# Performance work log

Measured on AMD Instinct MI355X. Metric: run time of the kernel, lower is better.

## Reference

```python
import jax, jax.numpy as jnp
import numpy as np

HID, OUT, D = 256, 64, 128
N_ITEM, N_USER, E = 100000, 50000, 800000


def sage_conv(x_src, x_dst, src, dst, w_l, b_l, w_r, n_dst):
    # PyG SAGEConv (mean aggr): out = lin_l(mean_j x_src[j]) + lin_r(x_dst)
    msg = x_src[src]                                        # [E, d_src] gather
    agg = jax.ops.segment_sum(msg, dst, num_segments=n_dst)  # [n_dst, d_src]
    cnt = jax.ops.segment_sum(jnp.ones((src.shape[0],), x_src.dtype), dst,
                              num_segments=n_dst)
    mean = agg / jnp.clip(cnt, 1.0, None)[:, None]
    return mean @ w_l + b_l + x_dst @ w_r


def setup_inputs() -> dict:
    key = jax.random.key(0)
    ks = jax.random.split(key, 16)
    sc = lambda d: 1.0 / np.sqrt(d)
    inp = {
        "x_item": jax.random.normal(ks[0], (N_ITEM, D), jnp.float32),
        "x_user": jax.random.normal(ks[1], (N_USER, D), jnp.float32),
        "ei_ii_src": jax.random.randint(ks[2], (E,), 0, N_ITEM),
        "ei_ii_dst": jax.random.randint(ks[3], (E,), 0, N_ITEM),
        "ei_iu_src": jax.random.randint(ks[4], (E,), 0, N_ITEM),
        "ei_iu_dst": jax.random.randint(ks[5], (E,), 0, N_USER),
        # conv1: item->item, in (D, D) -> HID
        "w_l1": jax.random.normal(ks[6], (D, HID), jnp.float32) * sc(D),
        "b1": jnp.zeros((HID,), jnp.float32),
        "w_r1": jax.random.normal(ks[7], (D, HID), jnp.float32) * sc(D),
        # conv2: (item D, user D) -> HID
        "w_l2": jax.random.normal(ks[8], (D, HID), jnp.float32) * sc(D),
        "b2": jnp.zeros((HID,), jnp.float32),
        "w_r2": jax.random.normal(ks[9], (D, HID), jnp.float32) * sc(D),
        # conv3: (item HID, user HID) -> HID
        "w_l3": jax.random.normal(ks[10], (HID, HID), jnp.float32) * sc(HID),
        "b3": jnp.zeros((HID,), jnp.float32),
        "w_r3": jax.random.normal(ks[11], (HID, HID), jnp.float32) * sc(HID),
        # final linear HID -> OUT
        "w_lin": jax.random.normal(ks[12], (HID, OUT), jnp.float32) * sc(HID),
        "b_lin": jnp.zeros((OUT,), jnp.float32),
    }
    return inp


def reference(x_item, x_user, ei_ii_src, ei_ii_dst, ei_iu_src, ei_iu_dst,
              w_l1, b1, w_r1, w_l2, b2, w_r2, w_l3, b3, w_r3, w_lin, b_lin):
    item_x = jax.nn.relu(sage_conv(x_item, x_item, ei_ii_src, ei_ii_dst,
                                   w_l1, b1, w_r1, N_ITEM))
    user_x = jax.nn.relu(sage_conv(x_item, x_user, ei_iu_src, ei_iu_dst,
                                   w_l2, b2, w_r2, N_USER))
    user_x = jax.nn.relu(sage_conv(item_x, user_x, ei_iu_src, ei_iu_dst,
                                   w_l3, b3, w_r3, N_USER))
    return user_x @ w_lin + b_lin
```

## Files before the change

### kernel.cpp

```cpp
#include <hip/hip_runtime.h>
#include <hip/hip_bf16.h>

#define N_ITEM 100000
#define N_USER 50000
#define D_IN   128
#define HID    256
#define OUT_D  64
#define CAP    64

#define SCB   782
#define CVIB  2048
#define CVUB  1024
#define PKB   136
#define PREP_GRID (SCB + CVIB + CVUB + PKB)

#define C2B   391
#define A3B   3125

typedef __attribute__((ext_vector_type(8))) short bf16x8;
typedef __attribute__((ext_vector_type(4))) float f32x4;

__device__ inline float b2f(unsigned int h) {
    union { unsigned int u; float f; } c; c.u = h << 16; return c.f;
}
__device__ inline unsigned short f2b(float f) {
    unsigned int u = __builtin_bit_cast(unsigned int, f);
    u += 0x7fff + ((u >> 16) & 1);
    return (unsigned short)(u >> 16);
}

__device__ inline void pack_unit(const float* __restrict__ wl,
                                 const float* __restrict__ wr,
                                 int K, int NCv, unsigned short* __restrict__ dst,
                                 int u)
{
    int kb = u / NCv, col = u - kb * NCv;
    int colp = col ^ (kb & 7);
    unsigned short tmp[8];
    #pragma unroll
    for (int j = 0; j < 8; ++j) {
        int k = kb * 8 + j;
        float w = (k < K) ? wl[(size_t)k * NCv + col]
                          : wr[(size_t)(k - K) * NCv + col];
        tmp[j] = f2b(w);
    }
    *(uint4*)&dst[((size_t)kb * NCv + colp) * 8] = *(const uint4*)tmp;
}

__global__ __launch_bounds__(256) void prep_kernel(
    const int* __restrict__ ii_src, const int* __restrict__ ii_dst,
    const int* __restrict__ iu_src, const int* __restrict__ iu_dst,
    int* __restrict__ cur_i, int* __restrict__ cur_u,
    int* __restrict__ slot_ii, int* __restrict__ slot_iu, int E,
    const float* __restrict__ x_item, const float* __restrict__ x_user,
    unsigned short* __restrict__ Acat1, unsigned short* __restrict__ Acat2,
    const float* __restrict__ wl1, const float* __restrict__ wr1,
    const float* __restrict__ wl2, const float* __restrict__ wr2,
    const float* __restrict__ wl3, const float* __restrict__ wr3,
    const float* __restrict__ wlin,
    unsigned short* __restrict__ Wp1, unsigned short* __restrict__ Wp2,
    unsigned short* __restrict__ Wp3, unsigned short* __restrict__ Wpl)
{
    int b = blockIdx.x;
    if (b < SCB) {
        int t = b * 256 + threadIdx.x;
        int e4 = t * 4;
        if (e4 + 3 < E) {
            int4 di = *(const int4*)&ii_dst[e4];
            int4 si = *(const int4*)&ii_src[e4];
            int4 du = *(const int4*)&iu_dst[e4];
            int4 su = *(const int4*)&iu_src[e4];
            int p0 = atomicAdd(&cur_i[di.x], 1);
            int p1 = atomicAdd(&cur_i[di.y], 1);
            int p2 = atomicAdd(&cur_i[di.z], 1);
            int p3 = atomicAdd(&cur_i[di.w], 1);
            int q0 = atomicAdd(&cur_u[du.x], 1);
            int q1 = atomicAdd(&cur_u[du.y], 1);
            int q2 = atomicAdd(&cur_u[du.z], 1);
            int q3 = atomicAdd(&cur_u[du.w], 1);
            if (p0 < CAP) slot_ii[di.x * CAP + p0] = si.x;
            if (p1 < CAP) slot_ii[di.y * CAP + p1] = si.y;
            if (p2 < CAP) slot_ii[di.z * CAP + p2] = si.z;
            if (p3 < CAP) slot_ii[di.w * CAP + p3] = si.w;
            if (q0 < CAP) slot_iu[du.x * CAP + q0] = su.x;
            if (q1 < CAP) slot_iu[du.y * CAP + q1] = su.y;
            if (q2 < CAP) slot_iu[du.z * CAP + q2] = su.z;
            if (q3 < CAP) slot_iu[du.w * CAP + q3] = su.w;
        } else {
            for (int e = e4; e < E; ++e) {
                int d0 = ii_dst[e], s0 = ii_src[e];
                int p = atomicAdd(&cur_i[d0], 1);
                if (p < CAP) slot_ii[d0 * CAP + p] = s0;
                int d1 = iu_dst[e], s1 = iu_src[e];
                int q = atomicAdd(&cur_u[d1], 1);
                if (q < CAP) slot_iu[d1 * CAP + q] = s1;
            }
        }
    } else if (b < SCB + CVIB) {
        const int STR = CVIB * 256;
        for (int u = (b - SCB) * 256 + threadIdx.x; u < N_ITEM * 32; u += STR) {
            int row = u >> 5, c4 = (u & 31) * 4;
            float4 v = *(const float4*)&x_item[(size_t)row * 128 + c4];
            ushort4 o;
            o.x = f2b(v.x); o.y = f2b(v.y); o.z = f2b(v.z); o.w = f2b(v.w);
            *(ushort4*)&Acat1[(size_t)row * 256 + 128 + c4] = o;
        }
    } else if (b < SCB + CVIB + CVUB) {
        const int STR = CVUB * 256;
        for (int u = (b - SCB - CVIB) * 256 + threadIdx.x; u < N_USER * 32; u += STR) {
            int row = u >> 5, c4 = (u & 31) * 4;
            float4 v = *(const float4*)&x_user[(size_t)row * 128 + c4];
            ushort4 o;
            o.x = f2b(v.x); o.y = f2b(v.y); o.z = f2b(v.z); o.w = f2b(v.w);
            *(ushort4*)&Acat2[(size_t)row * 256 + 128 + c4] = o;
        }
    } else {
        int t = (b - SCB - CVIB - CVUB) * 256 + threadIdx.x;
        if (t < 8192)       pack_unit(wl1, wr1, 128, 256, Wp1, t);
        else if (t < 16384) pack_unit(wl2, wr2, 128, 256, Wp2, t - 8192);
        else if (t < 32768) pack_unit(wl3, wr3, 256, 256, Wp3, t - 16384);
        else if (t < 34816) pack_unit(wlin, wlin, 256, 64, Wpl, t - 32768);
    }
}

__global__ __launch_bounds__(256) void agg12_kernel(
    const unsigned short* __restrict__ xsrc,
    const int* __restrict__ slot_ii, const int* __restrict__ cur_i,
    const int* __restrict__ slot_iu, const int* __restrict__ cur_u,
    unsigned short* __restrict__ Acat1, unsigned short* __restrict__ Acat2)
{
    int b = blockIdx.x;
    int sub = threadIdx.x >> 5;
    const int* sl; int num; unsigned short* dst;
    if (b < 12500) {
        int row = b * 8 + sub;
        sl  = slot_ii + (size_t)row * CAP;
        num = min(cur_i[row], CAP);
        dst = Acat1 + (size_t)row * 256;
    } else {
        int row = (b - 12500) * 8 + sub;
        sl  = slot_iu + (size_t)row * CAP;
        num = min(cur_u[row], CAP);
        dst = Acat2 + (size_t)row * 256;
    }
    int hl = threadIdx.x & 31;
    const unsigned short* xb = xsrc + hl * 4;
    float acc[4] = {};

    int j = 0;
    for (; j + 8 <= num; j += 8) {
        int s[8];
        #pragma unroll
        for (int u = 0; u < 8; ++u) s[u] = sl[j + u];
        uint2 v[8];
        #pragma unroll
        for (int u = 0; u < 8; ++u)
            v[u] = *(const uint2*)(xb + (size_t)s[u] * 256);
        #pragma unroll
        for (int u = 0; u < 8; ++u) {
            acc[0] += b2f(v[u].x & 0xffffu);
            acc[1] += b2f(v[u].x >> 16);
            acc[2] += b2f(v[u].y & 0xffffu);
            acc[3] += b2f(v[u].y >> 16);
        }
    }
    for (; j < num; ++j) {
        uint2 v = *(const uint2*)(xb + (size_t)sl[j] * 256);
        acc[0] += b2f(v.x & 0xffffu);
        acc[1] += b2f(v.x >> 16);
        acc[2] += b2f(v.y & 0xffffu);
        acc[3] += b2f(v.y >> 16);
    }

    float sc = 1.0f / fmaxf((float)num, 1.0f);
    uint2 w;
    w.x = (unsigned int)f2b(acc[0] * sc) | ((unsigned int)f2b(acc[1] * sc) << 16);
    w.y = (unsigned int)f2b(acc[2] * sc) | ((unsigned int)f2b(acc[3] * sc) << 16);
    *(uint2*)(dst + hl * 4) = w;
}

template <int NC, int WM, int WN, bool OUT_BF16, bool RELU>
__device__ __forceinline__ void gemm_body(
    int bid,
    const unsigned short* __restrict__ A, int lda,
    const unsigned short* __restrict__ Wp,
    const float* __restrict__ bias,
    void* __restrict__ Cout, int ldc, int col_off,
    int nrows, int nkt)
{
    constexpr int BM = 128;
    constexpr int MR = WM / 16, NR = WN / 16;
    constexpr int NWC = NC / WN;
    __shared__ unsigned short As[BM * 64];
    __shared__ unsigned short Bs[64 * NC];

    const int tid  = threadIdx.x;
    const int wave = tid >> 6;
    const int lane = tid & 63;
    const int row0 = bid * BM;
    const int wr = wave / NWC;
    const int wc = wave % NWC;

    f32x4 acc[MR][NR];
    #pragma unroll
    for (int m = 0; m < MR; ++m)
        #pragma unroll
        for (int n = 0; n < NR; ++n)
            acc[m][n] = (f32x4){0.f, 0.f, 0.f, 0.f};

    for (int kt = 0; kt < nkt; ++kt) {
        #pragma unroll
        for (int c = 0; c < 2; ++c) {
            int i = wave * 2 + c;
            int rl = 8 * i + (lane >> 3);
            int kc = (lane & 7) ^ (lane >> 3);
            const unsigned short* g =
                A + (size_t)(row0 + rl) * lda + kt * 64 + kc * 8;
            __builtin_amdgcn_global_load_lds(
                (const __attribute__((address_space(1))) void*)g,
                (__attribute__((address_space(3))) void*)(As + i * 512), 16, 0, 0);
        }
        constexpr int BCALLS = (64 * NC * 2) / 1024;
        constexpr int PW = BCALLS / 8;
        #pragma unroll
        for (int c = 0; c < PW; ++c) {
            int j = wave * PW + c;
            const unsigned short* g =
                Wp + (size_t)kt * (8 * NC * 8) + (size_t)j * 512 + lane * 8;
            __builtin_amdgcn_global_load_lds(
                (const __attribute__((address_space(1))) void*)g,
                (__attribute__((address_space(3))) void*)(Bs + j * 512), 16, 0, 0);
        }
        __syncthreads();

        #pragma unroll
        for (int kk = 0; kk < 2; ++kk) {
            bf16x8 af[MR], bfr[NR];
            #pragma unroll
            for (int m = 0; m < MR; ++m) {
                int row = wr * WM + m * 16 + (lane & 15);
                int kc = ((kk * 4) + (lane >> 4)) ^ (lane & 7);
                af[m] = *(const bf16x8*)(As + row * 64 + kc * 8);
            }
            #pragma unroll
            for (int n = 0; n < NR; ++n) {
                int kb = kk * 4 + (lane >> 4);
                int col = (wc * WN + n * 16 + (lane & 15)) ^ (kb & 7);
                bfr[n] = *(const bf16x8*)(Bs + (kb * NC + col) * 8);
            }
            #pragma unroll
            for (int m = 0; m < MR; ++m)
                #pragma unroll
                for (int n = 0; n < NR; ++n)
                    acc[m][n] = __builtin_amdgcn_mfma_f32_16x16x32_bf16(
                        af[m], bfr[n], acc[m][n], 0, 0, 0);
        }
        __syncthreads();
    }

    #pragma unroll
    for (int n = 0; n < NR; ++n) {
        int col = wc * WN + n * 16 + (lane & 15);
        float bv = bias[col];
        #pragma unroll
        for (int m = 0; m < MR; ++m) {
            #pragma unroll
            for (int j = 0; j < 4; ++j) {
                int row = row0 + wr * WM + m * 16 + (lane >> 4) * 4 + j;
                if (row < nrows) {
                    float v = acc[m][n][j] + bv;
                    if (RELU) v = fmaxf(v, 0.f);
                    if (OUT_BF16)
                        ((unsigned short*)Cout)[(size_t)row * ldc + col_off + col] = f2b(v);
                    else
                        ((float*)Cout)[(size_t)row * ldc + col_off + col] = v;
                }
            }
        }
    }
}

template <int NC, int WM, int WN, bool OUT_BF16, bool RELU>
__global__ __launch_bounds__(512) void gemm_mfma(
    const unsigned short* __restrict__ A, int lda,
    const unsigned short* __restrict__ Wp,
    const float* __restrict__ bias,
    void* __restrict__ Cout, int ldc, int col_off,
    int nrows, int nkt)
{
    gemm_body<NC, WM, WN, OUT_BF16, RELU>(blockIdx.x, A, lda, Wp, bias,
                                          Cout, ldc, col_off, nrows, nkt);
}

__global__ __launch_bounds__(512) void conv2_agg3_kernel(
    const unsigned short* __restrict__ Acat2,
    const unsigned short* __restrict__ Wp2,
    const float* __restrict__ b2,
    unsigned short* __restrict__ Acat3,
    const unsigned short* __restrict__ item_x,
    const int* __restrict__ slot_iu, const int* __restrict__ cur_u)
{
    if (blockIdx.x < C2B) {
        gemm_body<256, 64, 64, true, true>(blockIdx.x, Acat2, 256, Wp2, b2,
                                           Acat3, 512, 256, N_USER, 4);
        return;
    }
    int b = blockIdx.x - C2B;
    int row = b * 16 + (threadIdx.x >> 5);
    int hl = threadIdx.x & 31;
    const int* sl = slot_iu + (size_t)row * CAP;
    int num = min(cur_u[row], CAP);
    const unsigned short* xb = item_x + hl * 8;
    float acc[8] = {};

    int j = 0;
    for (; j + 8 <= num; j += 8) {
        int s[8];
        #pragma unroll
        for (int u = 0; u < 8; ++u) s[u] = sl[j + u];
        uint4 v[8];
        #pragma unroll
        for (int u = 0; u < 8; ++u)
            v[u] = *(const uint4*)(xb + (size_t)s[u] * 256);
        #pragma unroll
        for (int u = 0; u < 8; ++u) {
            acc[0] += b2f(v[u].x & 0xffffu);
            acc[1] += b2f(v[u].x >> 16);
            acc[2] += b2f(v[u].y & 0xffffu);
            acc[3] += b2f(v[u].y >> 16);
            acc[4] += b2f(v[u].z & 0xffffu);
            acc[5] += b2f(v[u].z >> 16);
            acc[6] += b2f(v[u].w & 0xffffu);
            acc[7] += b2f(v[u].w >> 16);
        }
    }
    for (; j < num; ++j) {
        uint4 v = *(const uint4*)(xb + (size_t)sl[j] * 256);
        acc[0] += b2f(v.x & 0xffffu);
        acc[1] += b2f(v.x >> 16);
        acc[2] += b2f(v.y & 0xffffu);
        acc[3] += b2f(v.y >> 16);
        acc[4] += b2f(v.z & 0xffffu);
        acc[5] += b2f(v.z >> 16);
        acc[6] += b2f(v.w & 0xffffu);
        acc[7] += b2f(v.w >> 16);
    }

    float sc = 1.0f / fmaxf((float)num, 1.0f);
    uint4 w;
    w.x = (unsigned int)f2b(acc[0] * sc) | ((unsigned int)f2b(acc[1] * sc) << 16);
    w.y = (unsigned int)f2b(acc[2] * sc) | ((unsigned int)f2b(acc[3] * sc) << 16);
    w.z = (unsigned int)f2b(acc[4] * sc) | ((unsigned int)f2b(acc[5] * sc) << 16);
    w.w = (unsigned int)f2b(acc[6] * sc) | ((unsigned int)f2b(acc[7] * sc) << 16);
    *(uint4*)(Acat3 + (size_t)row * 512 + hl * 8) = w;
}

extern "C" void kernel_launch(void* const* d_in, const int* in_sizes, int n_in,
                              void* d_out, int out_size, void* d_ws, size_t ws_size,
                              hipStream_t stream)
{
    const float* x_item = (const float*)d_in[0];
    const float* x_user = (const float*)d_in[1];
    const int* ii_src   = (const int*)d_in[2];
    const int* ii_dst   = (const int*)d_in[3];
    const int* iu_src   = (const int*)d_in[4];
    const int* iu_dst   = (const int*)d_in[5];
    const float* w_l1 = (const float*)d_in[6];
    const float* b1   = (const float*)d_in[7];
    const float* w_r1 = (const float*)d_in[8];
    const float* w_l2 = (const float*)d_in[9];
    const float* b2   = (const float*)d_in[10];
    const float* w_r2 = (const float*)d_in[11];
    const float* w_l3 = (const float*)d_in[12];
    const float* b3   = (const float*)d_in[13];
    const float* w_r3 = (const float*)d_in[14];
    const float* w_lin = (const float*)d_in[15];
    const float* b_lin = (const float*)d_in[16];
    float* out = (float*)d_out;

    const int E = in_sizes[2];
    const int NIP = 100096;
    const int NUP = 50048;

    int* cur_i   = (int*)d_ws;
    int* cur_u   = cur_i + 100352;
    int* slot_ii = cur_u + 50176;
    int* slot_iu = slot_ii + (size_t)N_ITEM * CAP;

    unsigned short* Acat1  = (unsigned short*)(slot_iu + (size_t)N_USER * CAP);
    unsigned short* item_x = Acat1  + (size_t)NIP * 256;
    unsigned short* Acat2  = item_x + (size_t)NIP * 256;
    unsigned short* Acat3  = Acat2  + (size_t)NUP * 256;
    unsigned short* ux3    = Acat3  + (size_t)NUP * 512;
    unsigned short* Wp1    = ux3    + (size_t)NUP * 256;
    unsigned short* Wp2    = Wp1 + 65536;
    unsigned short* Wp3    = Wp2 + 65536;
    unsigned short* Wpl    = Wp3 + 131072;

    hipMemsetAsync(cur_i, 0, (size_t)150528 * 4, stream);

    prep_kernel<<<PREP_GRID, 256, 0, stream>>>(
        ii_src, ii_dst, iu_src, iu_dst, cur_i, cur_u, slot_ii, slot_iu, E,
        x_item, x_user, Acat1, Acat2,
        w_l1, w_r1, w_l2, w_r2, w_l3, w_r3, w_lin,
        Wp1, Wp2, Wp3, Wpl);

    agg12_kernel<<<18750, 256, 0, stream>>>(
        Acat1 + 128, slot_ii, cur_i, slot_iu, cur_u, Acat1, Acat2);

    gemm_mfma<256, 64, 64, true, true><<<NIP / 128, 512, 0, stream>>>(
        Acat1, 256, Wp1, b1, item_x, 256, 0, N_ITEM, 4);

    conv2_agg3_kernel<<<C2B + A3B, 512, 0, stream>>>(
        Acat2, Wp2, b2, Acat3, item_x, slot_iu, cur_u);

    gemm_mfma<256, 64, 64, true, true><<<NUP / 128, 512, 0, stream>>>(
        Acat3, 512, Wp3, b3, ux3, 256, 0, N_USER, 8);

    gemm_mfma<64, 16, 64, false, false><<<NUP / 128, 512, 0, stream>>>(
        ux3, 256, Wpl, b_lin, out, 64, 0, N_USER, 4);
}
```

Measured before the change: 383.0 us.

## Restage pipeline to overlap iu scatter with item aggregation and conv1 with user aggregation

Splits the edge scatter into two stages. The item-user scatter now runs in the same launch as the item-item mean aggregation, and the item-user aggregation runs alongside the conv1 GEMM. Independent work is packed into shared grids so each launch has more concurrent blocks and there is less idle tail between dependent kernels. Launch count stays the same, but block sizes move to 512 threads. Packing GEMM blocks with gather blocks in one grid can cause imbalance or resource contention between the two kinds of blocks.

```diff
diff --git a/kernel.cpp b/kernel.cpp
--- a/kernel.cpp
+++ b/kernel.cpp
@@ -8,14 +8,23 @@
 #define OUT_D  64
 #define CAP    64
 
-#define SCB   782
-#define CVIB  2048
-#define CVUB  1024
-#define PKB   136
-#define PREP_GRID (SCB + CVIB + CVUB + PKB)
+#define S1B   391
+#define CV1B  1024
+#define CV2B  512
+#define PK1B  68
+#define G1 (S1B + CV1B + CV2B + PK1B)
+
+#define S2B   391
+#define A1B   6250
+#define G2 (S2B + A1B)
+
+#define C1B   782
+#define A2B   3125
+#define G3 (C1B + A2B)
 
 #define C2B   391
 #define A3B   3125
+#define G4 (C2B + A3B)
 
 typedef __attribute__((ext_vector_type(8))) short bf16x8;
 typedef __attribute__((ext_vector_type(4))) float f32x4;
@@ -27,6 +36,69 @@
     unsigned int u = __builtin_bit_cast(unsigned int, f);
     u += 0x7fff + ((u >> 16) & 1);
     return (unsigned short)(u >> 16);
+}
+
+__device__ __forceinline__ void scatter_body(
+    const int* __restrict__ src, const int* __restrict__ dstl,
+    int* __restrict__ cur, int* __restrict__ slot, int E, int t)
+{
+    int e4 = t * 4;
+    if (e4 + 3 < E) {
+        int4 d = *(const int4*)&dstl[e4];
+        int4 s = *(const int4*)&src[e4];
+        int p0 = atomicAdd(&cur[d.x], 1);
+        int p1 = atomicAdd(&cur[d.y], 1);
+        int p2 = atomicAdd(&cur[d.z], 1);
+        int p3 = atomicAdd(&cur[d.w], 1);
+        if (p0 < CAP) slot[d.x * CAP + p0] = s.x;
+        if (p1 < CAP) slot[d.y * CAP + p1] = s.y;
+        if (p2 < CAP) slot[d.z * CAP + p2] = s.z;
+        if (p3 < CAP) slot[d.w * CAP + p3] = s.w;
+    } else {
+        for (int e = e4; e < E; ++e) {
+            int d0 = dstl[e], s0 = src[e];
+            int p = atomicAdd(&cur[d0], 1);
+            if (p < CAP) slot[d0 * CAP + p] = s0;
+        }
+    }
+}
+
+__device__ __forceinline__ void agg_mean128_body(
+    const unsigned short* __restrict__ xsrc,
+    const int* __restrict__ sl, int num, int hl,
+    unsigned short* __restrict__ dstrow)
+{
+    const unsigned short* xb = xsrc + hl * 4;
+    float acc[4] = {};
+    int j = 0;
+    for (; j + 8 <= num; j += 8) {
+        int s[8];
+        #pragma unroll
+        for (int u = 0; u < 8; ++u) s[u] = sl[j + u];
+        uint2 v[8];
+        #pragma unroll
+        for (int u = 0; u < 8; ++u)
+            v[u] = *(const uint2*)(xb + (size_t)s[u] * 256);
+        #pragma unroll
+        for (int u = 0; u < 8; ++u) {
+            acc[0] += b2f(v[u].x & 0xffffu);
+            acc[1] += b2f(v[u].x >> 16);
+            acc[2] += b2f(v[u].y & 0xffffu);
+            acc[3] += b2f(v[u].y >> 16);
+        }
+    }
+    for (; j < num; ++j) {
+        uint2 v = *(const uint2*)(xb + (size_t)sl[j] * 256);
+        acc[0] += b2f(v.x & 0xffffu);
+        acc[1] += b2f(v.x >> 16);
+        acc[2] += b2f(v.y & 0xffffu);
+        acc[3] += b2f(v.y >> 16);
+    }
+    float sc = 1.0f / fmaxf((float)num, 1.0f);
+    uint2 w;
+    w.x = (unsigned int)f2b(acc[0] * sc) | ((unsigned int)f2b(acc[1] * sc) << 16);
+    w.y = (unsigned int)f2b(acc[2] * sc) | ((unsigned int)f2b(acc[3] * sc) << 16);
+    *(uint2*)(dstrow + hl * 4) = w;
 }
 
 __device__ inline void pack_unit(const float* __restrict__ wl,
@@ -47,11 +119,9 @@
     *(uint4*)&dst[((size_t)kb * NCv + colp) * 8] = *(const uint4*)tmp;
 }
 
-__global__ __launch_bounds__(256) void prep_kernel(
+__global__ __launch_bounds__(512) void prep1_kernel(
     const int* __restrict__ ii_src, const int* __restrict__ ii_dst,
-    const int* __restrict__ iu_src, const int* __restrict__ iu_dst,
-    int* __restrict__ cur_i, int* __restrict__ cur_u,
-    int* __restrict__ slot_ii, int* __restrict__ slot_iu, int E,
+    int* __restrict__ cur_i, int* __restrict__ slot_ii, int E,
     const float* __restrict__ x_item, const float* __restrict__ x_user,
     unsigned short* __restrict__ Acat1, unsigned short* __restrict__ Acat2,
     const float* __restrict__ wl1, const float* __restrict__ wr1,
@@ -62,52 +132,20 @@
     unsigned short* __restrict__ Wp3, unsigned short* __restrict__ Wpl)
 {
     int b = blockIdx.x;
-    if (b < SCB) {
-        int t = b * 256 + threadIdx.x;
-        int e4 = t * 4;
-        if (e4 + 3 < E) {
-            int4 di = *(const int4*)&ii_dst[e4];
-            int4 si = *(const int4*)&ii_src[e4];
-            int4 du = *(const int4*)&iu_dst[e4];
-            int4 su = *(const int4*)&iu_src[e4];
-            int p0 = atomicAdd(&cur_i[di.x], 1);
-            int p1 = atomicAdd(&cur_i[di.y], 1);
-            int p2 = atomicAdd(&cur_i[di.z], 1);
-            int p3 = atomicAdd(&cur_i[di.w], 1);
-            int q0 = atomicAdd(&cur_u[du.x], 1);
-            int q1 = atomicAdd(&cur_u[du.y], 1);
-            int q2 = atomicAdd(&cur_u[du.z], 1);
-            int q3 = atomicAdd(&cur_u[du.w], 1);
-            if (p0 < CAP) slot_ii[di.x * CAP + p0] = si.x;
-            if (p1 < CAP) slot_ii[di.y * CAP + p1] = si.y;
-            if (p2 < CAP) slot_ii[di.z * CAP + p2] = si.z;
-            if (p3 < CAP) slot_ii[di.w * CAP + p3] = si.w;
-            if (q0 < CAP) slot_iu[du.x * CAP + q0] = su.x;
-            if (q1 < CAP) slot_iu[du.y * CAP + q1] = su.y;
-            if (q2 < CAP) slot_iu[du.z * CAP + q2] = su.z;
-            if (q3 < CAP) slot_iu[du.w * CAP + q3] = su.w;
-        } else {
-            for (int e = e4; e < E; ++e) {
-                int d0 = ii_dst[e], s0 = ii_src[e];
-                int p = atomicAdd(&cur_i[d0], 1);
-                if (p < CAP) slot_ii[d0 * CAP + p] = s0;
-                int d1 = iu_dst[e], s1 = iu_src[e];
-                int q = atomicAdd(&cur_u[d1], 1);
-                if (q < CAP) slot_iu[d1 * CAP + q] = s1;
-            }
-        }
-    } else if (b < SCB + CVIB) {
-        const int STR = CVIB * 256;
-        for (int u = (b - SCB) * 256 + threadIdx.x; u < N_ITEM * 32; u += STR) {
+    if (b < S1B) {
+        scatter_body(ii_src, ii_dst, cur_i, slot_ii, E, b * 512 + threadIdx.x);
+    } else if (b < S1B + CV1B) {
+        const int STR = CV1B * 512;
+        for (int u = (b - S1B) * 512 + threadIdx.x; u < N_ITEM * 32; u += STR) {
             int row = u >> 5, c4 = (u & 31) * 4;
             float4 v = *(const float4*)&x_item[(size_t)row * 128 + c4];
             ushort4 o;
             o.x = f2b(v.x); o.y = f2b(v.y); o.z = f2b(v.z); o.w = f2b(v.w);
             *(ushort4*)&Acat1[(size_t)row * 256 + 128 + c4] = o;
         }
-    } else if (b < SCB + CVIB + CVUB) {
-        const int STR = CVUB * 256;
-        for (int u = (b - SCB - CVIB) * 256 + threadIdx.x; u < N_USER * 32; u += STR) {
+    } else if (b < S1B + CV1B + CV2B) {
+        const int STR = CV2B * 512;
+        for (int u = (b - S1B - CV1B) * 512 + threadIdx.x; u < N_USER * 32; u += STR) {
             int row = u >> 5, c4 = (u & 31) * 4;
             float4 v = *(const float4*)&x_user[(size_t)row * 128 + c4];
             ushort4 o;
@@ -115,7 +153,7 @@
             *(ushort4*)&Acat2[(size_t)row * 256 + 128 + c4] = o;
         }
     } else {
-        int t = (b - SCB - CVIB - CVUB) * 256 + threadIdx.x;
+        int t = (b - S1B - CV1B - CV2B) * 512 + threadIdx.x;
         if (t < 8192)       pack_unit(wl1, wr1, 128, 256, Wp1, t);
         else if (t < 16384) pack_unit(wl2, wr2, 128, 256, Wp2, t - 8192);
         else if (t < 32768) pack_unit(wl3, wr3, 256, 256, Wp3, t - 16384);
@@ -123,60 +161,23 @@
     }
 }
 
-__global__ __launch_bounds__(256) void agg12_kernel(
+__global__ __launch_bounds__(512) void prep2_kernel(
+    const int* __restrict__ iu_src, const int* __restrict__ iu_dst,
+    int* __restrict__ cur_u, int* __restrict__ slot_iu, int E,
     const unsigned short* __restrict__ xsrc,
     const int* __restrict__ slot_ii, const int* __restrict__ cur_i,
-    const int* __restrict__ slot_iu, const int* __restrict__ cur_u,
-    unsigned short* __restrict__ Acat1, unsigned short* __restrict__ Acat2)
+    unsigned short* __restrict__ Acat1)
 {
     int b = blockIdx.x;
-    int sub = threadIdx.x >> 5;
-    const int* sl; int num; unsigned short* dst;
-    if (b < 12500) {
-        int row = b * 8 + sub;
-        sl  = slot_ii + (size_t)row * CAP;
-        num = min(cur_i[row], CAP);
-        dst = Acat1 + (size_t)row * 256;
-    } else {
-        int row = (b - 12500) * 8 + sub;
-        sl  = slot_iu + (size_t)row * CAP;
-        num = min(cur_u[row], CAP);
-        dst = Acat2 + (size_t)row * 256;
-    }
+    if (b < S2B) {
+        scatter_body(iu_src, iu_dst, cur_u, slot_iu, E, b * 512 + threadIdx.x);
+        return;
+    }
+    int row = (b - S2B) * 16 + (threadIdx.x >> 5);
     int hl = threadIdx.x & 31;
-    const unsigned short* xb = xsrc + hl * 4;
-    float acc[4] = {};
-
-    int j = 0;
-    for (; j + 8 <= num; j += 8) {
-        int s[8];
-        #pragma unroll
-        for (int u = 0; u < 8; ++u) s[u] = sl[j + u];
-        uint2 v[8];
-        #pragma unroll
-        for (int u = 0; u < 8; ++u)
-            v[u] = *(const uint2*)(xb + (size_t)s[u] * 256);
-        #pragma unroll
-        for (int u = 0; u < 8; ++u) {
-            acc[0] += b2f(v[u].x & 0xffffu);
-            acc[1] += b2f(v[u].x >> 16);
-            acc[2] += b2f(v[u].y & 0xffffu);
-            acc[3] += b2f(v[u].y >> 16);
-        }
-    }
-    for (; j < num; ++j) {
-        uint2 v = *(const uint2*)(xb + (size_t)sl[j] * 256);
-        acc[0] += b2f(v.x & 0xffffu);
-        acc[1] += b2f(v.x >> 16);
-        acc[2] += b2f(v.y & 0xffffu);
-        acc[3] += b2f(v.y >> 16);
-    }
-
-    float sc = 1.0f / fmaxf((float)num, 1.0f);
-    uint2 w;
-    w.x = (unsigned int)f2b(acc[0] * sc) | ((unsigned int)f2b(acc[1] * sc) << 16);
-    w.y = (unsigned int)f2b(acc[2] * sc) | ((unsigned int)f2b(acc[3] * sc) << 16);
-    *(uint2*)(dst + hl * 4) = w;
+    const int* sl = slot_ii + (size_t)row * CAP;
+    int num = min(cur_i[row], CAP);
+    agg_mean128_body(xsrc, sl, num, hl, Acat1 + (size_t)row * 256);
 }
 
 template <int NC, int WM, int WN, bool OUT_BF16, bool RELU>
@@ -292,6 +293,28 @@
                                           Cout, ldc, col_off, nrows, nkt);
 }
 
+__global__ __launch_bounds__(512) void conv1_agg2_kernel(
+    const unsigned short* __restrict__ Acat1,
+    const unsigned short* __restrict__ Wp1,
+    const float* __restrict__ b1,
+    unsigned short* __restrict__ item_x,
+    const unsigned short* __restrict__ xsrc,
+    const int* __restrict__ slot_iu, const int* __restrict__ cur_u,
+    unsigned short* __restrict__ Acat2)
+{
+    if (blockIdx.x < C1B) {
+        gemm_body<256, 64, 64, true, true>(blockIdx.x, Acat1, 256, Wp1, b1,
+                                           item_x, 256, 0, N_ITEM, 4);
+        return;
+    }
+    int b = blockIdx.x - C1B;
+    int row = b * 16 + (threadIdx.x >> 5);
+    int hl = threadIdx.x & 31;
+    const int* sl = slot_iu + (size_t)row * CAP;
+    int num = min(cur_u[row], CAP);
+    agg_mean128_body(xsrc, sl, num, hl, Acat2 + (size_t)row * 256);
+}
+
 __global__ __launch_bounds__(512) void conv2_agg3_kernel(
     const unsigned short* __restrict__ Acat2,
     const unsigned short* __restrict__ Wp2,
@@ -399,19 +422,21 @@
 
     hipMemsetAsync(cur_i, 0, (size_t)150528 * 4, stream);
 
-    prep_kernel<<<PREP_GRID, 256, 0, stream>>>(
-        ii_src, ii_dst, iu_src, iu_dst, cur_i, cur_u, slot_ii, slot_iu, E,
+    prep1_kernel<<<G1, 512, 0, stream>>>(
+        ii_src, ii_dst, cur_i, slot_ii, E,
         x_item, x_user, Acat1, Acat2,
         w_l1, w_r1, w_l2, w_r2, w_l3, w_r3, w_lin,
         Wp1, Wp2, Wp3, Wpl);
 
-    agg12_kernel<<<18750, 256, 0, stream>>>(
-        Acat1 + 128, slot_ii, cur_i, slot_iu, cur_u, Acat1, Acat2);
-
-    gemm_mfma<256, 64, 64, true, true><<<NIP / 128, 512, 0, stream>>>(
-        Acat1, 256, Wp1, b1, item_x, 256, 0, N_ITEM, 4);
-
-    conv2_agg3_kernel<<<C2B + A3B, 512, 0, stream>>>(
+    prep2_kernel<<<G2, 512, 0, stream>>>(
+        iu_src, iu_dst, cur_u, slot_iu, E,
+        Acat1 + 128, slot_ii, cur_i, Acat1);
+
+    conv1_agg2_kernel<<<G3, 512, 0, stream>>>(
+        Acat1, Wp1, b1, item_x,
+        Acat1 + 128, slot_iu, cur_u, Acat2);
+
+    conv2_agg3_kernel<<<G4, 512, 0, stream>>>(
         Acat2, Wp2, b2, Acat3, item_x, slot_iu, cur_u);
 
     gemm_mfma<256, 64, 64, true, true><<<NUP / 128, 512, 0, stream>>>(
```

Measured after the change: 359.5 us. 6.1% less time.
